# Kernel optimization log

Measured on AMD Instinct MI355X. Metric: run time of the kernel, lower is better.

The kernel has to match this reference:

```python
import jax, jax.numpy as jnp
import numpy as np

B, S, D, E, K = 4, 4096, 2048, 64, 2

def setup_inputs() -> dict:
    key = jax.random.key(0)
    kx, kw = jax.random.split(key)
    x = jax.random.normal(kx, (B, S, D), dtype=jnp.float32)
    W = jax.random.normal(kw, (E, D), dtype=jnp.float32) * (1.0 / np.sqrt(D))
    b = jnp.zeros((E,), dtype=jnp.float32)
    return {"x": x, "W": W, "b": b, "k": K}

def reference(x, W, b, k):
    # logits: [B, S, E]
    logits = jnp.einsum('bsd,ed->bse', x, W) + b
    probs = jax.nn.softmax(logits, axis=-1)
    topk_probs, topk_experts = jax.lax.top_k(probs, k)  # [B,S,k]
    # one-hot over experts, OR-reduce over k -> bool mask [B,S,E]
    onehot = jax.nn.one_hot(topk_experts, E, dtype=jnp.int32)  # [B,S,k,E]
    masks = onehot.sum(axis=-2).astype(jnp.bool_)
    return (masks, probs)
```

## Files before the change

kernel.cpp:

```cpp
#include <hip/hip_runtime.h>
#include <math.h>

#define NTOK    16384
#define DDIM    2048
#define NEXP    64
#define PSTRIDE (NTOK * NEXP)
#define NPH     16
#define WSLICE  32768
#define XSLICE  32768

#define AS1 __attribute__((address_space(1)))
#define AS3 __attribute__((address_space(3)))

typedef _Float16 half8   __attribute__((ext_vector_type(8)));
typedef float    floatx4 __attribute__((ext_vector_type(4)));

__global__ __launch_bounds__(256) void wconv_kernel(
    const float* __restrict__ W, _Float16* __restrict__ ws)
{
    const int g     = blockIdx.x * 256 + threadIdx.x;
    const int p     = g >> 11;
    const int L     = g & 2047;
    const int plane = L >> 10;
    const int e     = (L >> 4) & 63;
    const int cp    = L & 15;
    const int c     = cp ^ (e & 7);
    const int k     = (p << 7) + (c << 3);

    const float* src = &W[(size_t)e * DDIM + k];
    floatx4 w0 = *(const floatx4*)src;
    floatx4 w1 = *(const floatx4*)(src + 4);

    half8 o;
#pragma unroll
    for (int i = 0; i < 4; ++i) {
        float f0 = w0[i], f1 = w1[i];
        _Float16 h0 = (_Float16)f0, h1 = (_Float16)f1;
        if (plane == 0) { o[i] = h0; o[4 + i] = h1; }
        else {
            o[i]     = (_Float16)((f0 - (float)h0) * 2048.0f);
            o[4 + i] = (_Float16)((f1 - (float)h1) * 2048.0f);
        }
    }
    *(half8*)((char*)ws + (size_t)g * 16) = o;
}

__global__ __launch_bounds__(512, 2) void router_kernel(
    const float* __restrict__ x,
    const _Float16* __restrict__ ws,
    const float* __restrict__ bias,
    float* __restrict__ out)
{
    __shared__ _Float16 lw[2][16384];
    __shared__ float    lx[2][8192];

    const int tid  = threadIdx.x;
    const int lane = tid & 63;
    const int wid  = tid >> 6;
    const int t    = wid >> 1;
    const int h    = wid & 1;
    const int t0b  = blockIdx.x * 64;
    const int t0   = t0b + t * 16;
    const int mrow = lane & 15;
    const int quad = lane >> 4;

    floatx4 acc_hh[4], acc_md[4];
#pragma unroll
    for (int j = 0; j < 4; ++j) { acc_hh[j] = (floatx4)0.0f; acc_md[j] = (floatx4)0.0f; }

    const char* gwp = (const char*)ws + wid * 4096 + lane * 16;
    const char* gxp[4];
#pragma unroll
    for (int i = 0; i < 4; ++i) {
        const int L   = wid * 256 + i * 64 + lane;
        const int row = L >> 5;
        const int c   = (L & 31) ^ (row & 7);
        gxp[i] = (const char*)x + (size_t)(t0b + row) * (DDIM * 4) + c * 16;
    }

#define STAGE(P, BUF)                                                          \
    {                                                                          \
        const char* gsw = gwp + (size_t)(P) * WSLICE;                          \
        char*       ldw = (char*)&lw[BUF][0] + wid * 4096;                     \
        _Pragma("unroll")                                                      \
        for (int i = 0; i < 4; ++i)                                            \
            __builtin_amdgcn_global_load_lds(                                  \
                (const AS1 unsigned int*)(const void*)(gsw + i * 1024),        \
                (AS3 unsigned int*)(void*)(ldw + i * 1024), 16, 0, 0);         \
        char* ldx = (char*)&lx[BUF][0] + wid * 4096;                           \
        _Pragma("unroll")                                                      \
        for (int i = 0; i < 4; ++i)                                            \
            __builtin_amdgcn_global_load_lds(                                  \
                (const AS1 unsigned int*)(const void*)(gxp[i] + (size_t)(P) * 512), \
                (AS3 unsigned int*)(void*)(ldx + i * 1024), 16, 0, 0);         \
    }

#define COMPUTE(BUF)                                                           \
    {                                                                          \
        const _Float16* wb   = &lw[BUF][0];                                    \
        const float*    xb   = &lx[BUF][0];                                    \
        const int       arow = t * 16 + mrow;                                  \
        _Pragma("unroll")                                                      \
        for (int s = 0; s < 2; ++s) {                                          \
            const int cc0 = h * 16 + s * 8 + quad * 2;                         \
            floatx4 X0 = *(const floatx4*)(xb + arow * 128 + ((cc0 ^ (arow & 7)) << 2)); \
            floatx4 X1 = *(const floatx4*)(xb + arow * 128 + (((cc0 + 1) ^ (arow & 7)) << 2)); \
            half8 a_hi, a_lo;                                                  \
            _Pragma("unroll")                                                  \
            for (int i = 0; i < 4; ++i) {                                      \
                float f0 = X0[i], f1 = X1[i];                                  \
                _Float16 h0 = (_Float16)f0, h1 = (_Float16)f1;                 \
                a_hi[i]     = h0; a_lo[i]     = (_Float16)((f0 - (float)h0) * 2048.0f); \
                a_hi[4 + i] = h1; a_lo[4 + i] = (_Float16)((f1 - (float)h1) * 2048.0f); \
            }                                                                  \
            _Pragma("unroll")                                                  \
            for (int j = 0; j < 4; ++j) {                                      \
                const int e   = j * 16 + mrow;                                 \
                const int ck  = h * 8 + s * 4 + quad;                          \
                const int off = e * 128 + ((ck ^ (e & 7)) << 3);               \
                half8 bh = *(const half8*)(wb + off);                          \
                half8 bl = *(const half8*)(wb + 8192 + off);                   \
                acc_hh[j] = __builtin_amdgcn_mfma_f32_16x16x32_f16(a_hi, bh, acc_hh[j], 0, 0, 0); \
                acc_md[j] = __builtin_amdgcn_mfma_f32_16x16x32_f16(a_hi, bl, acc_md[j], 0, 0, 0); \
                acc_md[j] = __builtin_amdgcn_mfma_f32_16x16x32_f16(a_lo, bh, acc_md[j], 0, 0, 0); \
            }                                                                  \
        }                                                                      \
    }

    STAGE(0, 0)

#pragma unroll 1
    for (int p = 0; p < NPH; ++p) {
        if (p < NPH - 1) {
            STAGE(p + 1, (p + 1) & 1)
            asm volatile("s_waitcnt vmcnt(8)" ::: "memory");
        } else {
            asm volatile("s_waitcnt vmcnt(0)" ::: "memory");
        }
        __builtin_amdgcn_s_barrier();
        asm volatile("" ::: "memory");
        COMPUTE(p & 1)
        __builtin_amdgcn_s_barrier();
        asm volatile("" ::: "memory");
    }

    float lg[4][4];
#pragma unroll
    for (int j = 0; j < 4; ++j)
#pragma unroll
        for (int r = 0; r < 4; ++r)
            lg[j][r] = acc_hh[j][r] + acc_md[j][r] * (1.0f / 2048.0f);

    float* rbuf = (float*)&lw[0][0];
    if (h == 1) {
#pragma unroll
        for (int j = 0; j < 4; ++j)
#pragma unroll
            for (int r = 0; r < 4; ++r)
                rbuf[t * 1024 + (j * 4 + r) * 64 + lane] = lg[j][r];
    }
    __syncthreads();
    if (h == 1) return;

#pragma unroll
    for (int j = 0; j < 4; ++j) {
        const float bj = bias[j * 16 + mrow];
#pragma unroll
        for (int r = 0; r < 4; ++r)
            lg[j][r] += rbuf[t * 1024 + (j * 4 + r) * 64 + lane] + bj;
    }

    const int c = mrow;
#pragma unroll
    for (int r = 0; r < 4; ++r) {
        const int trow = t0 + quad * 4 + r;

        float m = lg[0][r];
#pragma unroll
        for (int j = 1; j < 4; ++j) m = fmaxf(m, lg[j][r]);
#pragma unroll
        for (int off = 1; off <= 8; off <<= 1) m = fmaxf(m, __shfl_xor(m, off));

        float pj[4], s = 0.0f;
#pragma unroll
        for (int j = 0; j < 4; ++j) { pj[j] = __expf(lg[j][r] - m); s += pj[j]; }
#pragma unroll
        for (int off = 1; off <= 8; off <<= 1) s += __shfl_xor(s, off);
        const float rinv = 1.0f / s;

        float v1 = -1e30f, v2 = -1e30f; int i1 = -1, i2 = -1;
#pragma unroll
        for (int j = 0; j < 4; ++j) {
            float v = lg[j][r]; int e = j * 16 + c;
            if (v > v1 || (v == v1 && e < i1)) { v2 = v1; i2 = i1; v1 = v; i1 = e; }
            else if (v > v2 || (v == v2 && e < i2)) { v2 = v; i2 = e; }
        }
#pragma unroll
        for (int off = 1; off <= 8; off <<= 1) {
            float u1 = __shfl_xor(v1, off); int q1 = __shfl_xor(i1, off);
            float u2 = __shfl_xor(v2, off); int q2 = __shfl_xor(i2, off);
            if (u1 > v1 || (u1 == v1 && q1 < i1)) {
                if (v1 > u2 || (v1 == u2 && i1 < q2)) { v2 = v1; i2 = i1; }
                else                                   { v2 = u2; i2 = q2; }
                v1 = u1; i1 = q1;
            } else {
                if (u1 > v2 || (u1 == v2 && q1 < i2)) { v2 = u1; i2 = q1; }
            }
        }

#pragma unroll
        for (int j = 0; j < 4; ++j) {
            const int col = j * 16 + c;
            const size_t o = (size_t)trow * NEXP + col;
            out[o]           = (col == i1 || col == i2) ? 1.0f : 0.0f;
            out[PSTRIDE + o] = pj[j] * rinv;
        }
    }
}

extern "C" void kernel_launch(void* const* d_in, const int* in_sizes, int n_in,
                              void* d_out, int out_size, void* d_ws, size_t ws_size,
                              hipStream_t stream) {
    const float* x = (const float*)d_in[0];
    const float* W = (const float*)d_in[1];
    const float* b = (const float*)d_in[2];
    (void)in_sizes; (void)n_in; (void)out_size; (void)ws_size;
    float* out = (float*)d_out;

    _Float16* ws = (_Float16*)d_ws;

    hipLaunchKernelGGL(wconv_kernel, dim3(128), dim3(256), 0, stream, W, ws);
    hipLaunchKernelGGL(router_kernel, dim3(NTOK / 64), dim3(512), 0, stream, x, ws, b, out);
}
```

Measured before the change: 205.0 us.

## Split-K router GEMM across blocks with separate softmax/top-k finish kernel

Splits the 2048-long reduction into four K-ranges, each handled by its own block, so the grid grows from 256 to 1024 blocks of 256 threads and occupancy rises. x is now loaded straight into registers with a two-slot software pipeline, and only W goes through LDS. The GEMM writes fp32 partial logits to workspace. A new finish kernel sums the partials, adds bias and runs softmax and top-2 per token in a single thread. This trades under-filled CUs for extra partial-sum global traffic, one more launch, and a register-heavy per-thread finish step.

```diff
diff --git a/kernel.cpp b/kernel.cpp
--- a/kernel.cpp
+++ b/kernel.cpp
@@ -5,9 +5,11 @@
 #define DDIM    2048
 #define NEXP    64
 #define PSTRIDE (NTOK * NEXP)
-#define NPH     16
-#define WSLICE  32768
-#define XSLICE  32768
+#define KSPLIT  4
+#define KRANGE  512
+#define NPH     8
+#define WSLICE  16384
+#define PART_OFF (1 << 20)
 
 #define AS1 __attribute__((address_space(1)))
 #define AS3 __attribute__((address_space(3)))
@@ -19,13 +21,13 @@
     const float* __restrict__ W, _Float16* __restrict__ ws)
 {
     const int g     = blockIdx.x * 256 + threadIdx.x;
-    const int p     = g >> 11;
-    const int L     = g & 2047;
-    const int plane = L >> 10;
-    const int e     = (L >> 4) & 63;
-    const int cp    = L & 15;
+    const int p     = g >> 10;
+    const int L     = g & 1023;
+    const int plane = L >> 9;
+    const int e     = (L >> 3) & 63;
+    const int cp    = L & 7;
     const int c     = cp ^ (e & 7);
-    const int k     = (p << 7) + (c << 3);
+    const int k     = (p << 6) + (c << 3);
 
     const float* src = &W[(size_t)e * DDIM + k];
     floatx4 w0 = *(const floatx4*)src;
@@ -45,22 +47,19 @@
     *(half8*)((char*)ws + (size_t)g * 16) = o;
 }
 
-__global__ __launch_bounds__(512, 2) void router_kernel(
+__global__ __launch_bounds__(256, 4) void gemm_kernel(
     const float* __restrict__ x,
     const _Float16* __restrict__ ws,
-    const float* __restrict__ bias,
-    float* __restrict__ out)
+    float* __restrict__ part)
 {
-    __shared__ _Float16 lw[2][16384];
-    __shared__ float    lx[2][8192];
+    __shared__ _Float16 lw[2][8192];
 
     const int tid  = threadIdx.x;
     const int lane = tid & 63;
     const int wid  = tid >> 6;
-    const int t    = wid >> 1;
-    const int h    = wid & 1;
-    const int t0b  = blockIdx.x * 64;
-    const int t0   = t0b + t * 16;
+    const int sp   = blockIdx.x >> 8;
+    const int tg   = blockIdx.x & 255;
+    const int t0b  = tg * 64;
     const int mrow = lane & 15;
     const int quad = lane >> 4;
 
@@ -68,47 +67,40 @@
 #pragma unroll
     for (int j = 0; j < 4; ++j) { acc_hh[j] = (floatx4)0.0f; acc_md[j] = (floatx4)0.0f; }
 
-    const char* gwp = (const char*)ws + wid * 4096 + lane * 16;
-    const char* gxp[4];
-#pragma unroll
-    for (int i = 0; i < 4; ++i) {
-        const int L   = wid * 256 + i * 64 + lane;
-        const int row = L >> 5;
-        const int c   = (L & 31) ^ (row & 7);
-        gxp[i] = (const char*)x + (size_t)(t0b + row) * (DDIM * 4) + c * 16;
-    }
-
-#define STAGE(P, BUF)                                                          \
+    const char* gw0 = (const char*)ws + (size_t)(sp * NPH) * WSLICE
+                    + wid * 4096 + lane * 16;
+    const float* xrow = x + (size_t)(t0b + wid * 16 + mrow) * DDIM
+                      + sp * KRANGE + quad * 8;
+
+#define STAGE(Q, BUF)                                                          \
     {                                                                          \
-        const char* gsw = gwp + (size_t)(P) * WSLICE;                          \
+        const char* gsw = gw0 + (size_t)(Q) * WSLICE;                          \
         char*       ldw = (char*)&lw[BUF][0] + wid * 4096;                     \
         _Pragma("unroll")                                                      \
         for (int i = 0; i < 4; ++i)                                            \
             __builtin_amdgcn_global_load_lds(                                  \
                 (const AS1 unsigned int*)(const void*)(gsw + i * 1024),        \
                 (AS3 unsigned int*)(void*)(ldw + i * 1024), 16, 0, 0);         \
-        char* ldx = (char*)&lx[BUF][0] + wid * 4096;                           \
-        _Pragma("unroll")                                                      \
-        for (int i = 0; i < 4; ++i)                                            \
-            __builtin_amdgcn_global_load_lds(                                  \
-                (const AS1 unsigned int*)(const void*)(gxp[i] + (size_t)(P) * 512), \
-                (AS3 unsigned int*)(void*)(ldx + i * 1024), 16, 0, 0);         \
-    }
-
-#define COMPUTE(BUF)                                                           \
+    }
+
+#define LOADX(XV, Q)                                                           \
     {                                                                          \
-        const _Float16* wb   = &lw[BUF][0];                                    \
-        const float*    xb   = &lx[BUF][0];                                    \
-        const int       arow = t * 16 + mrow;                                  \
+        const float* xp = xrow + (Q) * 64;                                     \
+        XV[0] = *(const floatx4*)(xp);                                         \
+        XV[1] = *(const floatx4*)(xp + 4);                                     \
+        XV[2] = *(const floatx4*)(xp + 32);                                    \
+        XV[3] = *(const floatx4*)(xp + 36);                                    \
+    }
+
+#define COMPUTE(BUF, XV)                                                       \
+    {                                                                          \
+        const _Float16* wb = &lw[BUF][0];                                      \
         _Pragma("unroll")                                                      \
         for (int s = 0; s < 2; ++s) {                                          \
-            const int cc0 = h * 16 + s * 8 + quad * 2;                         \
-            floatx4 X0 = *(const floatx4*)(xb + arow * 128 + ((cc0 ^ (arow & 7)) << 2)); \
-            floatx4 X1 = *(const floatx4*)(xb + arow * 128 + (((cc0 + 1) ^ (arow & 7)) << 2)); \
             half8 a_hi, a_lo;                                                  \
             _Pragma("unroll")                                                  \
             for (int i = 0; i < 4; ++i) {                                      \
-                float f0 = X0[i], f1 = X1[i];                                  \
+                float f0 = XV[2 * s][i], f1 = XV[2 * s + 1][i];                \
                 _Float16 h0 = (_Float16)f0, h1 = (_Float16)f1;                 \
                 a_hi[i]     = h0; a_lo[i]     = (_Float16)((f0 - (float)h0) * 2048.0f); \
                 a_hi[4 + i] = h1; a_lo[4 + i] = (_Float16)((f1 - (float)h1) * 2048.0f); \
@@ -116,10 +108,10 @@
             _Pragma("unroll")                                                  \
             for (int j = 0; j < 4; ++j) {                                      \
                 const int e   = j * 16 + mrow;                                 \
-                const int ck  = h * 8 + s * 4 + quad;                          \
-                const int off = e * 128 + ((ck ^ (e & 7)) << 3);               \
+                const int ck  = s * 4 + quad;                                  \
+                const int off = e * 64 + ((ck ^ (e & 7)) << 3);                \
                 half8 bh = *(const half8*)(wb + off);                          \
-                half8 bl = *(const half8*)(wb + 8192 + off);                   \
+                half8 bl = *(const half8*)(wb + 4096 + off);                   \
                 acc_hh[j] = __builtin_amdgcn_mfma_f32_16x16x32_f16(a_hi, bh, acc_hh[j], 0, 0, 0); \
                 acc_md[j] = __builtin_amdgcn_mfma_f32_16x16x32_f16(a_hi, bl, acc_md[j], 0, 0, 0); \
                 acc_md[j] = __builtin_amdgcn_mfma_f32_16x16x32_f16(a_lo, bh, acc_md[j], 0, 0, 0); \
@@ -127,94 +119,97 @@
         }                                                                      \
     }
 
+    floatx4 xa[4], xb[4];
+
     STAGE(0, 0)
+    LOADX(xa, 0)
 
 #pragma unroll 1
-    for (int p = 0; p < NPH; ++p) {
-        if (p < NPH - 1) {
-            STAGE(p + 1, (p + 1) & 1)
+    for (int q = 0; q < NPH; q += 2) {
+        STAGE(q + 1, 1)
+        LOADX(xb, q + 1)
+        asm volatile("s_waitcnt vmcnt(8)" ::: "memory");
+        __builtin_amdgcn_s_barrier();
+        asm volatile("" ::: "memory");
+        COMPUTE(0, xa)
+        __builtin_amdgcn_s_barrier();
+        asm volatile("" ::: "memory");
+
+        if (q < NPH - 2) {
+            STAGE(q + 2, 0)
+            LOADX(xa, q + 2)
             asm volatile("s_waitcnt vmcnt(8)" ::: "memory");
         } else {
             asm volatile("s_waitcnt vmcnt(0)" ::: "memory");
         }
         __builtin_amdgcn_s_barrier();
         asm volatile("" ::: "memory");
-        COMPUTE(p & 1)
-        __builtin_amdgcn_s_barrier();
-        asm volatile("" ::: "memory");
-    }
-
-    float lg[4][4];
+        COMPUTE(1, xb)
+        __builtin_amdgcn_s_barrier();
+        asm volatile("" ::: "memory");
+    }
+
+    float* pb = part + (size_t)sp * PSTRIDE;
 #pragma unroll
     for (int j = 0; j < 4; ++j)
 #pragma unroll
-        for (int r = 0; r < 4; ++r)
-            lg[j][r] = acc_hh[j][r] + acc_md[j][r] * (1.0f / 2048.0f);
-
-    float* rbuf = (float*)&lw[0][0];
-    if (h == 1) {
-#pragma unroll
-        for (int j = 0; j < 4; ++j)
-#pragma unroll
-            for (int r = 0; r < 4; ++r)
-                rbuf[t * 1024 + (j * 4 + r) * 64 + lane] = lg[j][r];
-    }
-    __syncthreads();
-    if (h == 1) return;
-
-#pragma unroll
-    for (int j = 0; j < 4; ++j) {
-        const float bj = bias[j * 16 + mrow];
-#pragma unroll
-        for (int r = 0; r < 4; ++r)
-            lg[j][r] += rbuf[t * 1024 + (j * 4 + r) * 64 + lane] + bj;
-    }
-
-    const int c = mrow;
-#pragma unroll
-    for (int r = 0; r < 4; ++r) {
-        const int trow = t0 + quad * 4 + r;
-
-        float m = lg[0][r];
-#pragma unroll
-        for (int j = 1; j < 4; ++j) m = fmaxf(m, lg[j][r]);
-#pragma unroll
-        for (int off = 1; off <= 8; off <<= 1) m = fmaxf(m, __shfl_xor(m, off));
-
-        float pj[4], s = 0.0f;
-#pragma unroll
-        for (int j = 0; j < 4; ++j) { pj[j] = __expf(lg[j][r] - m); s += pj[j]; }
-#pragma unroll
-        for (int off = 1; off <= 8; off <<= 1) s += __shfl_xor(s, off);
-        const float rinv = 1.0f / s;
-
-        float v1 = -1e30f, v2 = -1e30f; int i1 = -1, i2 = -1;
-#pragma unroll
-        for (int j = 0; j < 4; ++j) {
-            float v = lg[j][r]; int e = j * 16 + c;
-            if (v > v1 || (v == v1 && e < i1)) { v2 = v1; i2 = i1; v1 = v; i1 = e; }
-            else if (v > v2 || (v == v2 && e < i2)) { v2 = v; i2 = e; }
-        }
-#pragma unroll
-        for (int off = 1; off <= 8; off <<= 1) {
-            float u1 = __shfl_xor(v1, off); int q1 = __shfl_xor(i1, off);
-            float u2 = __shfl_xor(v2, off); int q2 = __shfl_xor(i2, off);
-            if (u1 > v1 || (u1 == v1 && q1 < i1)) {
-                if (v1 > u2 || (v1 == u2 && i1 < q2)) { v2 = v1; i2 = i1; }
-                else                                   { v2 = u2; i2 = q2; }
-                v1 = u1; i1 = q1;
-            } else {
-                if (u1 > v2 || (u1 == v2 && q1 < i2)) { v2 = u1; i2 = q1; }
-            }
-        }
-
-#pragma unroll
-        for (int j = 0; j < 4; ++j) {
-            const int col = j * 16 + c;
-            const size_t o = (size_t)trow * NEXP + col;
-            out[o]           = (col == i1 || col == i2) ? 1.0f : 0.0f;
-            out[PSTRIDE + o] = pj[j] * rinv;
-        }
+        for (int r = 0; r < 4; ++r) {
+            const float v = acc_hh[j][r] + acc_md[j][r] * (1.0f / 2048.0f);
+            const int trow = t0b + wid * 16 + quad * 4 + r;
+            pb[(size_t)trow * NEXP + j * 16 + mrow] = v;
+        }
+}
+
+__global__ __launch_bounds__(64) void finish_kernel(
+    const float* __restrict__ part,
+    const float* __restrict__ bias,
+    float* __restrict__ out)
+{
+    const int t = blockIdx.x * 64 + threadIdx.x;
+    const float* p0 = part + (size_t)t * NEXP;
+
+    float lg[NEXP];
+#pragma unroll
+    for (int c = 0; c < 16; ++c) {
+        floatx4 v = *(const floatx4*)(p0 + c * 4);
+#pragma unroll
+        for (int sp = 1; sp < KSPLIT; ++sp)
+            v += *(const floatx4*)(p0 + (size_t)sp * PSTRIDE + c * 4);
+        v += *(const floatx4*)(bias + c * 4);
+#pragma unroll
+        for (int i = 0; i < 4; ++i) lg[c * 4 + i] = v[i];
+    }
+
+    float m = lg[0];
+#pragma unroll
+    for (int e = 1; e < NEXP; ++e) m = fmaxf(m, lg[e]);
+
+    float pr[NEXP], s = 0.0f;
+#pragma unroll
+    for (int e = 0; e < NEXP; ++e) { pr[e] = __expf(lg[e] - m); s += pr[e]; }
+    const float rinv = 1.0f / s;
+
+    float v1 = -1e30f, v2 = -1e30f; int i1 = -1, i2 = -1;
+#pragma unroll
+    for (int e = 0; e < NEXP; ++e) {
+        const float v = lg[e];
+        if (v > v1)      { v2 = v1; i2 = i1; v1 = v; i1 = e; }
+        else if (v > v2) { v2 = v;  i2 = e; }
+    }
+
+    float* om = out + (size_t)t * NEXP;
+    float* op = out + PSTRIDE + (size_t)t * NEXP;
+#pragma unroll
+    for (int c = 0; c < 16; ++c) {
+        floatx4 mv, pv;
+#pragma unroll
+        for (int i = 0; i < 4; ++i) {
+            const int e = c * 4 + i;
+            mv[i] = (e == i1 || e == i2) ? 1.0f : 0.0f;
+            pv[i] = pr[e] * rinv;
+        }
+        *(floatx4*)(om + c * 4) = mv;
+        *(floatx4*)(op + c * 4) = pv;
     }
 }
 
@@ -227,8 +222,10 @@
     (void)in_sizes; (void)n_in; (void)out_size; (void)ws_size;
     float* out = (float*)d_out;
 
-    _Float16* ws = (_Float16*)d_ws;
+    _Float16* ws   = (_Float16*)d_ws;
+    float*    part = (float*)((char*)d_ws + PART_OFF);
 
     hipLaunchKernelGGL(wconv_kernel, dim3(128), dim3(256), 0, stream, W, ws);
-    hipLaunchKernelGGL(router_kernel, dim3(NTOK / 64), dim3(512), 0, stream, x, ws, b, out);
-}
+    hipLaunchKernelGGL(gemm_kernel, dim3(256 * KSPLIT), dim3(256), 0, stream, x, ws, part);
+    hipLaunchKernelGGL(finish_kernel, dim3(NTOK / 64), dim3(64), 0, stream, part, b, out);
+}
```

Result: slower. 212.9 us (+3.9%).

## Split router GEMM over K into partial sums with separate softmax/top-k kernel

Applied to the files above, without the earlier changes.

Restructures the router into a split-K GEMM: 512 blocks each handle 128 tokens over a 512-wide K range, writing fp32 partial logits to workspace. A new finish kernel sums the four partials, adds bias and does softmax/top-2 masking. The weight layout and swizzle are rebuilt for 32-wide K phases, and each block reuses its W fragments across two token tiles. This is meant to raise parallelism and LDS efficiency beyond the 256-block grid, at the cost of an extra launch and partial-sum traffic.

```diff
diff --git a/kernel.cpp b/kernel.cpp
--- a/kernel.cpp
+++ b/kernel.cpp
@@ -5,9 +5,12 @@
 #define DDIM    2048
 #define NEXP    64
 #define PSTRIDE (NTOK * NEXP)
+#define KSPLIT  4
+#define KRANGE  512
 #define NPH     16
-#define WSLICE  32768
-#define XSLICE  32768
+#define TOKB    128
+#define WSLICE  8192
+#define PART_OFF (1 << 20)
 
 #define AS1 __attribute__((address_space(1)))
 #define AS3 __attribute__((address_space(3)))
@@ -19,13 +22,13 @@
     const float* __restrict__ W, _Float16* __restrict__ ws)
 {
     const int g     = blockIdx.x * 256 + threadIdx.x;
-    const int p     = g >> 11;
-    const int L     = g & 2047;
-    const int plane = L >> 10;
-    const int e     = (L >> 4) & 63;
-    const int cp    = L & 15;
-    const int c     = cp ^ (e & 7);
-    const int k     = (p << 7) + (c << 3);
+    const int p     = g >> 9;
+    const int L     = g & 511;
+    const int plane = L >> 8;
+    const int e     = (L >> 2) & 63;
+    const int cp    = L & 3;
+    const int c     = cp ^ (e & 3);
+    const int k     = (p << 5) + (c << 3);
 
     const float* src = &W[(size_t)e * DDIM + k];
     floatx4 w0 = *(const floatx4*)src;
@@ -45,66 +48,80 @@
     *(half8*)((char*)ws + (size_t)g * 16) = o;
 }
 
-__global__ __launch_bounds__(512, 2) void router_kernel(
+__global__ __launch_bounds__(256, 2) void gemm_kernel(
     const float* __restrict__ x,
     const _Float16* __restrict__ ws,
-    const float* __restrict__ bias,
-    float* __restrict__ out)
+    float* __restrict__ part)
 {
-    __shared__ _Float16 lw[2][16384];
-    __shared__ float    lx[2][8192];
+    __shared__ _Float16 lw[2][4096];
+    __shared__ float    lx[2][4096];
 
     const int tid  = threadIdx.x;
     const int lane = tid & 63;
     const int wid  = tid >> 6;
-    const int t    = wid >> 1;
-    const int h    = wid & 1;
-    const int t0b  = blockIdx.x * 64;
-    const int t0   = t0b + t * 16;
+    const int sp   = blockIdx.x >> 7;
+    const int tg   = blockIdx.x & 127;
+    const int t0b  = tg * TOKB;
     const int mrow = lane & 15;
     const int quad = lane >> 4;
 
-    floatx4 acc_hh[4], acc_md[4];
-#pragma unroll
-    for (int j = 0; j < 4; ++j) { acc_hh[j] = (floatx4)0.0f; acc_md[j] = (floatx4)0.0f; }
-
-    const char* gwp = (const char*)ws + wid * 4096 + lane * 16;
-    const char* gxp[4];
+    floatx4 acc_hh[2][4], acc_md[2][4];
+#pragma unroll
+    for (int tt = 0; tt < 2; ++tt)
+#pragma unroll
+        for (int j = 0; j < 4; ++j) {
+            acc_hh[tt][j] = (floatx4)0.0f;
+            acc_md[tt][j] = (floatx4)0.0f;
+        }
+
+    const char* gw0 = (const char*)ws + (size_t)(sp * NPH) * WSLICE
+                    + wid * 2048 + lane * 16;
+    const char* gx[4];
 #pragma unroll
     for (int i = 0; i < 4; ++i) {
         const int L   = wid * 256 + i * 64 + lane;
-        const int row = L >> 5;
-        const int c   = (L & 31) ^ (row & 7);
-        gxp[i] = (const char*)x + (size_t)(t0b + row) * (DDIM * 4) + c * 16;
-    }
-
-#define STAGE(P, BUF)                                                          \
+        const int row = L >> 3;
+        const int c   = (L & 7) ^ (row & 7);
+        gx[i] = (const char*)x + (size_t)(t0b + row) * (DDIM * 4)
+              + sp * (KRANGE * 4) + c * 16;
+    }
+
+#define STAGE(Q, BUF)                                                          \
     {                                                                          \
-        const char* gsw = gwp + (size_t)(P) * WSLICE;                          \
-        char*       ldw = (char*)&lw[BUF][0] + wid * 4096;                     \
-        _Pragma("unroll")                                                      \
-        for (int i = 0; i < 4; ++i)                                            \
-            __builtin_amdgcn_global_load_lds(                                  \
-                (const AS1 unsigned int*)(const void*)(gsw + i * 1024),        \
-                (AS3 unsigned int*)(void*)(ldw + i * 1024), 16, 0, 0);         \
+        const char* gsw = gw0 + (size_t)(Q) * WSLICE;                          \
+        char*       ldw = (char*)&lw[BUF][0] + wid * 2048;                     \
+        __builtin_amdgcn_global_load_lds(                                      \
+            (const AS1 unsigned int*)(const void*)(gsw),                       \
+            (AS3 unsigned int*)(void*)(ldw), 16, 0, 0);                        \
+        __builtin_amdgcn_global_load_lds(                                      \
+            (const AS1 unsigned int*)(const void*)(gsw + 1024),               \
+            (AS3 unsigned int*)(void*)(ldw + 1024), 16, 0, 0);                 \
         char* ldx = (char*)&lx[BUF][0] + wid * 4096;                           \
         _Pragma("unroll")                                                      \
         for (int i = 0; i < 4; ++i)                                            \
             __builtin_amdgcn_global_load_lds(                                  \
-                (const AS1 unsigned int*)(const void*)(gxp[i] + (size_t)(P) * 512), \
+                (const AS1 unsigned int*)(const void*)(gx[i] + (size_t)(Q) * 128), \
                 (AS3 unsigned int*)(void*)(ldx + i * 1024), 16, 0, 0);         \
     }
 
 #define COMPUTE(BUF)                                                           \
     {                                                                          \
-        const _Float16* wb   = &lw[BUF][0];                                    \
-        const float*    xb   = &lx[BUF][0];                                    \
-        const int       arow = t * 16 + mrow;                                  \
+        const _Float16* wb = &lw[BUF][0];                                      \
+        const float*    xb = &lx[BUF][0];                                      \
+        half8 bh[4], bl[4];                                                    \
         _Pragma("unroll")                                                      \
-        for (int s = 0; s < 2; ++s) {                                          \
-            const int cc0 = h * 16 + s * 8 + quad * 2;                         \
-            floatx4 X0 = *(const floatx4*)(xb + arow * 128 + ((cc0 ^ (arow & 7)) << 2)); \
-            floatx4 X1 = *(const floatx4*)(xb + arow * 128 + (((cc0 + 1) ^ (arow & 7)) << 2)); \
+        for (int j = 0; j < 4; ++j) {                                          \
+            const int e   = j * 16 + mrow;                                     \
+            const int off = e * 32 + ((quad ^ (e & 3)) << 3);                  \
+            bh[j] = *(const half8*)(wb + off);                                 \
+            bl[j] = *(const half8*)(wb + 2048 + off);                          \
+        }                                                                      \
+        _Pragma("unroll")                                                      \
+        for (int tt = 0; tt < 2; ++tt) {                                       \
+            const int arow = (wid + tt * 4) * 16 + mrow;                       \
+            const int c0   = quad * 2;                                         \
+            floatx4 X0 = *(const floatx4*)(xb + arow * 32 + ((c0 ^ (arow & 7)) << 2)); \
+            floatx4 X1 = *(const floatx4*)(xb + arow * 32 + (((c0 + 1) ^ (arow & 7)) << 2)); \
             half8 a_hi, a_lo;                                                  \
             _Pragma("unroll")                                                  \
             for (int i = 0; i < 4; ++i) {                                      \
@@ -115,14 +132,9 @@
             }                                                                  \
             _Pragma("unroll")                                                  \
             for (int j = 0; j < 4; ++j) {                                      \
-                const int e   = j * 16 + mrow;                                 \
-                const int ck  = h * 8 + s * 4 + quad;                          \
-                const int off = e * 128 + ((ck ^ (e & 7)) << 3);               \
-                half8 bh = *(const half8*)(wb + off);                          \
-                half8 bl = *(const half8*)(wb + 8192 + off);                   \
-                acc_hh[j] = __builtin_amdgcn_mfma_f32_16x16x32_f16(a_hi, bh, acc_hh[j], 0, 0, 0); \
-                acc_md[j] = __builtin_amdgcn_mfma_f32_16x16x32_f16(a_hi, bl, acc_md[j], 0, 0, 0); \
-                acc_md[j] = __builtin_amdgcn_mfma_f32_16x16x32_f16(a_lo, bh, acc_md[j], 0, 0, 0); \
+                acc_hh[tt][j] = __builtin_amdgcn_mfma_f32_16x16x32_f16(a_hi, bh[j], acc_hh[tt][j], 0, 0, 0); \
+                acc_md[tt][j] = __builtin_amdgcn_mfma_f32_16x16x32_f16(a_hi, bl[j], acc_md[tt][j], 0, 0, 0); \
+                acc_md[tt][j] = __builtin_amdgcn_mfma_f32_16x16x32_f16(a_lo, bh[j], acc_md[tt][j], 0, 0, 0); \
             }                                                                  \
         }                                                                      \
     }
@@ -130,50 +142,64 @@
     STAGE(0, 0)
 
 #pragma unroll 1
-    for (int p = 0; p < NPH; ++p) {
-        if (p < NPH - 1) {
-            STAGE(p + 1, (p + 1) & 1)
-            asm volatile("s_waitcnt vmcnt(8)" ::: "memory");
+    for (int q = 0; q < NPH; ++q) {
+        if (q < NPH - 1) {
+            STAGE(q + 1, (q + 1) & 1)
+            asm volatile("s_waitcnt vmcnt(6)" ::: "memory");
         } else {
             asm volatile("s_waitcnt vmcnt(0)" ::: "memory");
         }
         __builtin_amdgcn_s_barrier();
         asm volatile("" ::: "memory");
-        COMPUTE(p & 1)
+        COMPUTE(q & 1)
         __builtin_amdgcn_s_barrier();
         asm volatile("" ::: "memory");
     }
 
+    float* pb = part + (size_t)sp * PSTRIDE;
+#pragma unroll
+    for (int tt = 0; tt < 2; ++tt) {
+        const int tl = tg * 8 + wid + tt * 4;
+#pragma unroll
+        for (int j = 0; j < 4; ++j) {
+            floatx4 v;
+#pragma unroll
+            for (int r = 0; r < 4; ++r)
+                v[r] = acc_hh[tt][j][r] + acc_md[tt][j][r] * (1.0f / 2048.0f);
+            *(floatx4*)(pb + (size_t)tl * 1024 + j * 256 + lane * 4) = v;
+        }
+    }
+}
+
+__global__ __launch_bounds__(256) void finish_kernel(
+    const float* __restrict__ part,
+    const float* __restrict__ bias,
+    float* __restrict__ out)
+{
+    const int tid  = threadIdx.x;
+    const int lane = tid & 63;
+    const int wid  = tid >> 6;
+    const int tl   = blockIdx.x * 4 + wid;
+    const int mrow = lane & 15;
+    const int quad = lane >> 4;
+
     float lg[4][4];
 #pragma unroll
-    for (int j = 0; j < 4; ++j)
-#pragma unroll
-        for (int r = 0; r < 4; ++r)
-            lg[j][r] = acc_hh[j][r] + acc_md[j][r] * (1.0f / 2048.0f);
-
-    float* rbuf = (float*)&lw[0][0];
-    if (h == 1) {
-#pragma unroll
-        for (int j = 0; j < 4; ++j)
-#pragma unroll
-            for (int r = 0; r < 4; ++r)
-                rbuf[t * 1024 + (j * 4 + r) * 64 + lane] = lg[j][r];
-    }
-    __syncthreads();
-    if (h == 1) return;
-
-#pragma unroll
     for (int j = 0; j < 4; ++j) {
+        floatx4 v = *(const floatx4*)(part + (size_t)tl * 1024 + j * 256 + lane * 4);
+#pragma unroll
+        for (int sp = 1; sp < KSPLIT; ++sp)
+            v += *(const floatx4*)(part + (size_t)sp * PSTRIDE
+                                   + (size_t)tl * 1024 + j * 256 + lane * 4);
         const float bj = bias[j * 16 + mrow];
 #pragma unroll
-        for (int r = 0; r < 4; ++r)
-            lg[j][r] += rbuf[t * 1024 + (j * 4 + r) * 64 + lane] + bj;
+        for (int r = 0; r < 4; ++r) lg[j][r] = v[r] + bj;
     }
 
     const int c = mrow;
 #pragma unroll
     for (int r = 0; r < 4; ++r) {
-        const int trow = t0 + quad * 4 + r;
+        const int trow = tl * 16 + quad * 4 + r;
 
         float m = lg[0][r];
 #pragma unroll
@@ -227,8 +253,10 @@
     (void)in_sizes; (void)n_in; (void)out_size; (void)ws_size;
     float* out = (float*)d_out;
 
-    _Float16* ws = (_Float16*)d_ws;
+    _Float16* ws   = (_Float16*)d_ws;
+    float*    part = (float*)((char*)d_ws + PART_OFF);
 
     hipLaunchKernelGGL(wconv_kernel, dim3(128), dim3(256), 0, stream, W, ws);
-    hipLaunchKernelGGL(router_kernel, dim3(NTOK / 64), dim3(512), 0, stream, x, ws, b, out);
-}
+    hipLaunchKernelGGL(gemm_kernel, dim3(128 * KSPLIT), dim3(256), 0, stream, x, ws, part);
+    hipLaunchKernelGGL(finish_kernel, dim3(256), dim3(256), 0, stream, part, b, out);
+}
```

Measured after the change: 215.9 us. +5.4%, slower.
